# Kernel optimization log

Hardware: AMD Instinct MI355X
Metric: run time of the kernel (lower is better)

Reference implementation:

```python
import jax, jax.numpy as jnp
import numpy as np

N_NODES = 10000
N_EDGES = 160000


def setup_inputs() -> dict:
    key = jax.random.key(0)
    ks = jax.random.split(key, 12)
    B, N, DIN, DH, DOUT, L = 8, N_NODES, 512, 256, 3, 6
    s = lambda *d: 1.0 / np.sqrt(d[-2])
    return {
        "x": jax.random.normal(ks[0], (B, N, DIN), jnp.float32),
        "edge_src": jax.random.randint(ks[1], (N_EDGES,), 0, N, jnp.int32),
        "edge_dst": jax.random.randint(ks[2], (N_EDGES,), 0, N, jnp.int32),
        "edge_w": jax.random.uniform(ks[3], (N_EDGES,), jnp.float32) / 16.0,  # ~row-normalized
        "W_in": jax.random.normal(ks[4], (DIN, DH), jnp.float32) * s(DIN, DH),
        "LW_in": jax.random.normal(ks[5], (DIN, DH), jnp.float32) * s(DIN, DH),
        "b_in": jnp.zeros((DH,), jnp.float32),
        "W_blk": jax.random.normal(ks[6], (L, 2, DH, DH), jnp.float32) * s(DH, DH),
        "LW_blk": jax.random.normal(ks[7], (L, 2, DH, DH), jnp.float32) * s(DH, DH),
        "b_blk": jnp.zeros((L, 2, DH), jnp.float32),
        "W_out": jax.random.normal(ks[8], (DH, DOUT), jnp.float32) * s(DH, DOUT),
        "LW_out": jax.random.normal(ks[9], (DH, DOUT), jnp.float32) * s(DH, DOUT),
        "b_out": jnp.zeros((DOUT,), jnp.float32),
    }


def _gconv(x, esrc, edst, ew, W, LW, b):
    # x: [B,N,Din] -> [B,N,Dout]; out = A @ (x W) + x LW + b with sparse A
    support = jnp.einsum("bnd,de->bne", x, W)
    msgs = support[:, esrc, :] * ew[None, :, None]          # [B,E,Do]
    agg = jax.ops.segment_sum(msgs.transpose(1, 0, 2), edst,
                              num_segments=x.shape[1])       # [N,B,Do]
    agg = agg.transpose(1, 0, 2)                             # [B,N,Do]
    return agg + jnp.einsum("bnd,de->bne", x, LW) + b


def reference(x, edge_src, edge_dst, edge_w, W_in, LW_in, b_in,
              W_blk, LW_blk, b_blk, W_out, LW_out, b_out):
    h = _gconv(x, edge_src, edge_dst, edge_w, W_in, LW_in, b_in)
    for l in range(W_blk.shape[0]):  # GResBlock: two GConvs, residual, *0.5
        t = _gconv(h, edge_src, edge_dst, edge_w, W_blk[l, 0], LW_blk[l, 0], b_blk[l, 0])
        t = _gconv(t, edge_src, edge_dst, edge_w, W_blk[l, 1], LW_blk[l, 1], b_blk[l, 1])
        h = (h + t) * 0.5
    x_out = _gconv(h, edge_src, edge_dst, edge_w, W_out, LW_out, b_out)
    return (x_out, h)
```

## Files before the change

### kernel.cpp

```cpp
#include <hip/hip_runtime.h>

#define NN 10000
#define BB 8
#define MROWS 80000

typedef float f32x4 __attribute__((ext_vector_type(4)));
typedef unsigned int u32x4 __attribute__((ext_vector_type(4)));
typedef _Float16 f16;
typedef _Float16 f16x8 __attribute__((ext_vector_type(8)));

typedef __attribute__((address_space(1))) void as1_void;
typedef __attribute__((address_space(3))) void as3_void;

static __device__ __forceinline__ void gl_lds16(const void* g, void* l){
  __builtin_amdgcn_global_load_lds((as1_void*)g, (as3_void*)l, 16, 0, 0);
}

__global__ void k_count(const int* __restrict__ dst, int E, int* __restrict__ counts){
  int i = blockIdx.x * blockDim.x + threadIdx.x;
  if(i < E) atomicAdd(&counts[dst[i]], 1);
}

__global__ void k_scan(const int* __restrict__ counts, int* __restrict__ rp2){
  __shared__ int buf[1024];
  __shared__ int carry;
  const int t = threadIdx.x;
  if(t == 0){ carry = 0; rp2[0] = 0; }
  __syncthreads();
  for(int base = 0; base < NN; base += 1024){
    int v = (base + t < NN) ? ((counts[base + t] + 1) & ~1) : 0;
    buf[t] = v;
    __syncthreads();
    for(int off = 1; off < 1024; off <<= 1){
      int x = (t >= off) ? buf[t - off] : 0;
      __syncthreads();
      buf[t] += x;
      __syncthreads();
    }
    if(base + t < NN) rp2[base + t + 1] = carry + buf[t];
    __syncthreads();
    if(t == 0) carry += buf[1023];
    __syncthreads();
  }
}

__global__ void k_fill(const int* __restrict__ dst, int E, const int* __restrict__ rp2,
                       int* __restrict__ cursor, int* __restrict__ ci){
  int i = blockIdx.x * blockDim.x + threadIdx.x;
  if(i < E){
    int d = dst[i];
    int p = rp2[d] + atomicAdd(&cursor[d], 1);
    ci[p] = i;
  }
}

__global__ void k_sort_rows(const int* __restrict__ rp2, const int* __restrict__ cursor,
                            int* __restrict__ ci, unsigned int* __restrict__ ev,
                            const int* __restrict__ esrc, const float* __restrict__ ew){
  const int n = blockIdx.x * blockDim.x + threadIdx.x;
  if(n >= NN) return;
  const int s = rp2[n];
  const int deg = cursor[n];
  const int e = s + deg;
  for(int i = s; i < e - 1; ++i){
    int mj = i, mv = ci[i];
    for(int j = i + 1; j < e; ++j){
      int v = ci[j];
      if(v < mv){ mv = v; mj = j; }
    }
    ci[mj] = ci[i]; ci[i] = mv;
  }
  for(int p = s; p < e; ++p){
    int eid = ci[p];
    ev[2 * p]     = (unsigned int)esrc[eid];
    ev[2 * p + 1] = __float_as_uint(ew[eid]);
  }
  const int e2 = rp2[n + 1];
  for(int p = e; p < e2; ++p){
    ev[2 * p]     = 0u;
    ev[2 * p + 1] = 0u;
  }
}

__global__ void k_cvt(const float4* __restrict__ in, f16x8* __restrict__ out, int n8){
  int i = blockIdx.x * blockDim.x + threadIdx.x;
  if(i >= n8) return;
  float4 v0 = in[2 * i], v1 = in[2 * i + 1];
  f16x8 o;
  o[0] = (f16)v0.x; o[1] = (f16)v0.y; o[2] = (f16)v0.z; o[3] = (f16)v0.w;
  o[4] = (f16)v1.x; o[5] = (f16)v1.y; o[6] = (f16)v1.z; o[7] = (f16)v1.w;
  out[i] = o;
}

__global__ void k_pack_w(const float* __restrict__ Wi, const float* __restrict__ LWi,
                         const float* __restrict__ Wb, const float* __restrict__ LWb,
                         f16* __restrict__ dh){
  const int T0 = 512 * 512;
  const int TOT = T0 + 12 * 512 * 256;
  int i = blockIdx.x * blockDim.x + threadIdx.x;
  if(i >= TOT) return;
  float v;
  if(i < T0){
    int c = i >> 9, k = i & 511;
    v = (c < 256) ? Wi[k * 256 + c] : LWi[k * 256 + (c - 256)];
  } else {
    int j = i - T0;
    int li = j >> 17;
    int r = j & 131071;
    int c = r >> 8, k = r & 255;
    const float* src = (c < 256) ? (Wb + (size_t)li * 65536) : (LWb + (size_t)li * 65536);
    v = src[k * 256 + (c & 255)];
  }
  dh[i] = (f16)v;
}

__global__ __launch_bounds__(256) void k_gemm_dual(
    const f16* __restrict__ A, const f16* __restrict__ Bt,
    f16* __restrict__ Sup, f16* __restrict__ Loc, int K, int nblk)
{
  __shared__ char smem[40960];
  const int t = threadIdx.x;
  const int pid = blockIdx.x;
  const int q = nblk >> 3, r = nblk & 7;
  const int xcd = pid & 7, sl = pid >> 3;
  const int wg = (xcd < r ? xcd * (q + 1) : r * (q + 1) + (xcd - r) * q) + sl;
  const int m0 = (wg >> 1) << 6;
  const int by = wg & 1;
  const int n0 = by << 8;
  const int lane = t & 63, wv = t >> 6;
  const int rA = lane & 15, g = lane >> 4;
  f32x4 acc[4][4] = {};
  const int nsteps = K >> 5;
  const int rowt = t >> 2;
  const int csw  = (t & 3) ^ ((rowt >> 1) & 3);
  const int cbt  = csw << 3;

  auto STAGE = [&](int s, int buf){
    const int k0 = s << 5;
    const size_t aoff = (size_t)(m0 + rowt) * K + k0 + cbt;
    gl_lds16(A + aoff, smem + buf * 4096 + t * 16);
    #pragma unroll
    for(int qq = 0; qq < 4; ++qq){
      const size_t boff = (size_t)(n0 + qq * 64 + rowt) * K + k0 + cbt;
      gl_lds16(Bt + boff, smem + 8192 + buf * 16384 + qq * 4096 + t * 16);
    }
  };

  STAGE(0, 0);
  int cur = 0;
  const int slotx = (rA >> 1) & 3;

  for(int s = 0; s < nsteps; ++s){
    __builtin_amdgcn_sched_barrier(0);
    if(s + 1 < nsteps){
      STAGE(s + 1, cur ^ 1);
      asm volatile("s_waitcnt vmcnt(5)" ::: "memory");
    } else {
      asm volatile("s_waitcnt vmcnt(0)" ::: "memory");
    }
    __builtin_amdgcn_s_barrier();
    __builtin_amdgcn_sched_barrier(0);

    f16x8 av[4], bv[4];
    const f16* AsC = (const f16*)(smem + cur * 4096);
    const f16* BsC = (const f16*)(smem + 8192 + cur * 16384);
    #pragma unroll
    for(int mi = 0; mi < 4; ++mi){
      const int ao = (mi * 16 + rA) * 32 + ((g ^ slotx) << 3);
      av[mi] = *(const f16x8*)(AsC + ao);
    }
    #pragma unroll
    for(int ni = 0; ni < 4; ++ni){
      const int bo = wv * 2048 + (ni * 16 + rA) * 32 + ((g ^ slotx) << 3);
      bv[ni] = *(const f16x8*)(BsC + bo);
    }
    #pragma unroll
    for(int mi = 0; mi < 4; ++mi){
      #pragma unroll
      for(int ni = 0; ni < 4; ++ni){
        acc[mi][ni] = __builtin_amdgcn_mfma_f32_16x16x32_f16(av[mi], bv[ni], acc[mi][ni], 0, 0, 0);
      }
    }
    __builtin_amdgcn_sched_barrier(0);
    __builtin_amdgcn_s_barrier();
    cur ^= 1;
  }

  __syncthreads();
  f16* bounce = (f16*)smem;
  const int SP = 264;
  const int wn = wv << 6;
  #pragma unroll
  for(int mi = 0; mi < 4; ++mi){
    #pragma unroll
    for(int ni = 0; ni < 4; ++ni){
      const int col = wn + ni * 16 + rA;
      #pragma unroll
      for(int r2 = 0; r2 < 4; ++r2){
        bounce[(mi * 16 + g * 4 + r2) * SP + col] = (f16)acc[mi][ni][r2];
      }
    }
  }
  __syncthreads();
  f16* dstp = ((by == 0) ? Sup : Loc) + (size_t)m0 * 256;
  #pragma unroll
  for(int rr = 0; rr < 8; ++rr){
    const int e = rr * 2048 + t * 8;
    const int row = e >> 8, col = e & 255;
    const f16x8 v = *(const f16x8*)(bounce + row * SP + col);
    *(f16x8*)(dstp + e) = v;
  }
}

__global__ __launch_bounds__(256) void k_agg_q(
    const f16* __restrict__ Sup, const f16* __restrict__ Loc,
    const float* __restrict__ bias,
    const int* __restrict__ rp2, const unsigned int* __restrict__ ev,
    const f16* __restrict__ Hprev, f16* __restrict__ Hnext,
    float* __restrict__ hout, const int mode)
{
  const int pid = blockIdx.x;
  const int b = pid & 7;
  const int rest = pid >> 3;
  const int grp = rest % 313;
  const int qd  = rest / 313;
  const int t = threadIdx.x;
  const int j = t >> 3;
  const int l = t & 7;
  const int n = grp * 32 + j;
  if(n >= NN) return;
  const int d0 = (qd << 6) + (l << 3);
  const size_t rb = ((size_t)b * NN + n) * 256 + d0;
  float a[8];
  {
    const f16x8 lv = *(const f16x8*)(Loc + rb);
    float4 q0 = *(const float4*)(bias + d0);
    float4 q1 = *(const float4*)(bias + d0 + 4);
    a[0] = (float)lv[0] + q0.x; a[1] = (float)lv[1] + q0.y;
    a[2] = (float)lv[2] + q0.z; a[3] = (float)lv[3] + q0.w;
    a[4] = (float)lv[4] + q1.x; a[5] = (float)lv[5] + q1.y;
    a[6] = (float)lv[6] + q1.z; a[7] = (float)lv[7] + q1.w;
  }
  const int s = rp2[n], e = rp2[n + 1];
  const size_t bb = (size_t)b * NN * 256 + d0;
  for(int i = s; i < e; i += 2){
    const u32x4 ee = *(const u32x4*)(ev + 2 * i);
    const float w0 = __uint_as_float(ee[1]);
    const float w1 = __uint_as_float(ee[3]);
    const f16x8 h0 = *(const f16x8*)(Sup + bb + ((size_t)(int)ee[0]) * 256);
    const f16x8 h1 = *(const f16x8*)(Sup + bb + ((size_t)(int)ee[2]) * 256);
    #pragma unroll
    for(int d = 0; d < 8; ++d){
      a[d] = fmaf(w0, (float)h0[d], a[d]);
      a[d] = fmaf(w1, (float)h1[d], a[d]);
    }
  }
  if(mode >= 2){
    const f16x8 hp = *(const f16x8*)(Hprev + rb);
    #pragma unroll
    for(int d = 0; d < 8; ++d) a[d] = (a[d] + (float)hp[d]) * 0.5f;
  }
  if(mode == 3){
    f32x4 o0 = {a[0], a[1], a[2], a[3]};
    f32x4 o1 = {a[4], a[5], a[6], a[7]};
    *(f32x4*)(hout + rb) = o0;
    *(f32x4*)(hout + rb + 4) = o1;
    return;
  }
  f16x8 o;
  #pragma unroll
  for(int d = 0; d < 8; ++d) o[d] = (f16)a[d];
  *(f16x8*)(Hnext + rb) = o;
}

__global__ __launch_bounds__(256) void k_out_sup(const float* __restrict__ h,
    const float* __restrict__ Wo, float* __restrict__ sup3){
  const int gid = blockIdx.x * 4 + (threadIdx.x >> 6);
  const int lane = threadIdx.x & 63;
  if(gid >= MROWS) return;
  const float4 v = *(const float4*)(h + (size_t)gid * 256 + lane * 4);
  const float hv[4] = {v.x, v.y, v.z, v.w};
  float p0 = 0.f, p1 = 0.f, p2 = 0.f;
  #pragma unroll
  for(int j = 0; j < 4; ++j){
    const int k = lane * 4 + j;
    p0 = fmaf(hv[j], Wo[k * 3 + 0], p0);
    p1 = fmaf(hv[j], Wo[k * 3 + 1], p1);
    p2 = fmaf(hv[j], Wo[k * 3 + 2], p2);
  }
  #pragma unroll
  for(int off = 32; off; off >>= 1){
    p0 += __shfl_xor(p0, off, 64);
    p1 += __shfl_xor(p1, off, 64);
    p2 += __shfl_xor(p2, off, 64);
  }
  if(lane == 0){
    float* o = sup3 + (size_t)gid * 3;
    o[0] = p0; o[1] = p1; o[2] = p2;
  }
}

__global__ __launch_bounds__(256) void k_out_final(const float* __restrict__ h,
    const float* __restrict__ LWo, const float* __restrict__ bo,
    const int* __restrict__ rp2, const unsigned int* __restrict__ ev,
    const float* __restrict__ sup3, float* __restrict__ out){
  const int gid = blockIdx.x * 4 + (threadIdx.x >> 6);
  const int lane = threadIdx.x & 63;
  if(gid >= MROWS) return;
  const int b = gid / NN, n = gid % NN;
  const float4 v = *(const float4*)(h + (size_t)gid * 256 + lane * 4);
  const float hv[4] = {v.x, v.y, v.z, v.w};
  float p0 = 0.f, p1 = 0.f, p2 = 0.f;
  #pragma unroll
  for(int j = 0; j < 4; ++j){
    const int k = lane * 4 + j;
    p0 = fmaf(hv[j], LWo[k * 3 + 0], p0);
    p1 = fmaf(hv[j], LWo[k * 3 + 1], p1);
    p2 = fmaf(hv[j], LWo[k * 3 + 2], p2);
  }
  const int s = rp2[n], e = rp2[n + 1];
  for(int i = s + lane; i < e; i += 64){
    const int src = (int)ev[2 * i];
    const float w = __uint_as_float(ev[2 * i + 1]);
    const float* sp = sup3 + ((size_t)b * NN + src) * 3;
    p0 = fmaf(w, sp[0], p0);
    p1 = fmaf(w, sp[1], p1);
    p2 = fmaf(w, sp[2], p2);
  }
  #pragma unroll
  for(int off = 32; off; off >>= 1){
    p0 += __shfl_xor(p0, off, 64);
    p1 += __shfl_xor(p1, off, 64);
    p2 += __shfl_xor(p2, off, 64);
  }
  if(lane == 0){
    float* o = out + (size_t)gid * 3;
    o[0] = p0 + bo[0]; o[1] = p1 + bo[1]; o[2] = p2 + bo[2];
  }
}

extern "C" void kernel_launch(void* const* d_in, const int* in_sizes, int n_in,
                              void* d_out, int out_size, void* d_ws, size_t ws_size,
                              hipStream_t stream) {
  const float* x     = (const float*)d_in[0];
  const int*   esrc  = (const int*)d_in[1];
  const int*   edst  = (const int*)d_in[2];
  const float* ew    = (const float*)d_in[3];
  const float* W_in  = (const float*)d_in[4];
  const float* LW_in = (const float*)d_in[5];
  const float* b_in  = (const float*)d_in[6];
  const float* W_blk = (const float*)d_in[7];
  const float* LW_blk= (const float*)d_in[8];
  const float* b_blk = (const float*)d_in[9];
  const float* W_out = (const float*)d_in[10];
  const float* LW_out= (const float*)d_in[11];
  const float* b_out = (const float*)d_in[12];
  const int E = in_sizes[1];

  float* outF  = (float*)d_out;
  float* xout  = outF;
  float* hOut  = outF + 240000;
  f16* x16 = (f16*)hOut;

  char* ws = (char*)d_ws;
  size_t off = 0;
  auto alloc = [&](size_t bytes) -> char* {
    char* p = ws + off;
    off += (bytes + 255) & ~(size_t)255;
    return p;
  };
  const size_t HB = (size_t)20480000 * 2;
  f16* Ha  = (f16*)alloc(HB);
  f16* Hb  = (f16*)alloc(HB);
  f16* Sup = (f16*)alloc(HB);
  f16* Loc = (f16*)alloc(HB);
  const int WTOT = 512 * 512 + 12 * 512 * 256;
  f16* Wt = (f16*)alloc((size_t)WTOT * 2);
  float* sup3    = (float*)alloc((size_t)240000 * 4);
  int*   counts  = (int*)alloc((size_t)2 * NN * 4);
  int*   cursor  = counts + NN;
  int*   rp2     = (int*)alloc((size_t)(NN + 1) * 4);
  int*   ci      = (int*)alloc((size_t)(E + NN) * 4);
  unsigned int* ev = (unsigned int*)alloc((size_t)2 * (E + NN) * 4);
  (void)ws_size; (void)n_in; (void)out_size;

  hipMemsetAsync(counts, 0, (size_t)2 * NN * 4, stream);
  k_count<<<(E + 255) / 256, 256, 0, stream>>>(edst, E, counts);
  k_scan<<<1, 1024, 0, stream>>>(counts, rp2);
  k_fill<<<(E + 255) / 256, 256, 0, stream>>>(edst, E, rp2, cursor, ci);
  k_sort_rows<<<(NN + 255) / 256, 256, 0, stream>>>(rp2, cursor, ci, ev, esrc, ew);

  k_cvt<<<(5120000 + 255) / 256, 256, 0, stream>>>((const float4*)x, (f16x8*)x16, 5120000);
  k_pack_w<<<(WTOT + 255) / 256, 256, 0, stream>>>(W_in, LW_in, W_blk, LW_blk, Wt);

  const int NBLK = 2500;
  const int ABLK = 10016;
  k_gemm_dual<<<NBLK, 256, 0, stream>>>(x16, Wt, Sup, Loc, 512, NBLK);
  k_agg_q<<<ABLK, 256, 0, stream>>>(Sup, Loc, b_in, rp2, ev, Ha, Ha, xout, 0);

  const f16* Wm = Wt + 512 * 512;
  for(int l = 0; l < 6; ++l){
    const int li0 = 2 * l, li1 = 2 * l + 1;
    k_gemm_dual<<<NBLK, 256, 0, stream>>>(Ha, Wm + (size_t)li0 * 131072, Sup, Loc, 256, NBLK);
    k_agg_q<<<ABLK, 256, 0, stream>>>(Sup, Loc, b_blk + li0 * 256, rp2, ev, Ha, Hb, xout, 0);
    k_gemm_dual<<<NBLK, 256, 0, stream>>>(Hb, Wm + (size_t)li1 * 131072, Sup, Loc, 256, NBLK);
    k_agg_q<<<ABLK, 256, 0, stream>>>(Sup, Loc, b_blk + li1 * 256, rp2, ev, Ha, Ha, hOut, (l == 5) ? 3 : 2);
  }

  k_out_sup<<<MROWS / 4, 256, 0, stream>>>(hOut, W_out, sup3);
  k_out_final<<<MROWS / 4, 256, 0, stream>>>(hOut, LW_out, b_out, rp2, ev, sup3, xout);
}
```

Before: 1.464 ms.

## Add register-resident weight GEMM kernel for hidden-layer graph convolutions

Adds a persistent GEMM kernel for the 256-wide hidden layers. Each wave keeps a 64-column strip of the combined W|LW weight matrix in registers (32 f16x8 vectors) and loops over 16-row tiles of the activations. Results go through a small per-wave LDS bounce so the stores to Sup/Loc are coalesced. This removes the per-tile LDS staging and block-level syncs of the old dual GEMM. In exchange it uses much more register space, which lowers occupancy, and every wave reloads each A tile from global memory with no sharing across the 8 strips.

```diff
diff --git a/kernel.cpp b/kernel.cpp
--- a/kernel.cpp
+++ b/kernel.cpp
@@ -209,6 +209,66 @@
     const int row = e >> 8, col = e & 255;
     const f16x8 v = *(const f16x8*)(bounce + row * SP + col);
     *(f16x8*)(dstp + e) = v;
+  }
+}
+
+__global__ __launch_bounds__(256) void k_gemm_regB(
+    const f16* __restrict__ A, const f16* __restrict__ Bt,
+    f16* __restrict__ Sup, f16* __restrict__ Loc)
+{
+  __shared__ f16 bnc[4][16 * 72];
+  const int t = threadIdx.x;
+  const int wv = t >> 6, lane = t & 63;
+  const int gw = blockIdx.x * 4 + wv;
+  const int strip = gw & 7;
+  const int chunk = gw >> 3;
+  const int rA = lane & 15, g = lane >> 4;
+  f16* dst = (strip < 4) ? Sup : Loc;
+  const int dc0 = (strip & 3) << 6;
+
+  f16x8 breg[32];
+  {
+    const f16* bp = Bt + (size_t)((strip << 6) + rA) * 256 + g * 8;
+    #pragma unroll
+    for(int tt = 0; tt < 4; ++tt){
+      #pragma unroll
+      for(int ss = 0; ss < 8; ++ss){
+        breg[tt * 8 + ss] = *(const f16x8*)(bp + (size_t)tt * 16 * 256 + ss * 32);
+      }
+    }
+  }
+
+  const int rowrd = lane >> 2;
+  const int colrd = (lane & 3) << 4;
+  f16* mybnc = bnc[wv];
+
+  for(int mt = chunk; mt < 5000; mt += 256){
+    const f16* ap = A + (size_t)(mt * 16 + rA) * 256 + g * 8;
+    f16x8 av[8];
+    #pragma unroll
+    for(int ss = 0; ss < 8; ++ss) av[ss] = *(const f16x8*)(ap + ss * 32);
+    f32x4 acc[4] = {};
+    #pragma unroll
+    for(int ss = 0; ss < 8; ++ss){
+      #pragma unroll
+      for(int tt = 0; tt < 4; ++tt){
+        acc[tt] = __builtin_amdgcn_mfma_f32_16x16x32_f16(av[ss], breg[tt * 8 + ss], acc[tt], 0, 0, 0);
+      }
+    }
+    #pragma unroll
+    for(int tt = 0; tt < 4; ++tt){
+      #pragma unroll
+      for(int r2 = 0; r2 < 4; ++r2){
+        mybnc[(g * 4 + r2) * 72 + tt * 16 + rA] = (f16)acc[tt][r2];
+      }
+    }
+    asm volatile("s_waitcnt lgkmcnt(0)" ::: "memory");
+    const f16x8 v0 = *(const f16x8*)(mybnc + rowrd * 72 + colrd);
+    const f16x8 v1 = *(const f16x8*)(mybnc + rowrd * 72 + colrd + 8);
+    f16* dp = dst + (size_t)(mt * 16 + rowrd) * 256 + dc0 + colrd;
+    *(f16x8*)dp = v0;
+    *(f16x8*)(dp + 8) = v1;
+    asm volatile("s_waitcnt lgkmcnt(0)" ::: "memory");
   }
 }
 
@@ -394,6 +454,7 @@
   k_pack_w<<<(WTOT + 255) / 256, 256, 0, stream>>>(W_in, LW_in, W_blk, LW_blk, Wt);
 
   const int NBLK = 2500;
+  const int GBLK = 512;
   const int ABLK = 10016;
   k_gemm_dual<<<NBLK, 256, 0, stream>>>(x16, Wt, Sup, Loc, 512, NBLK);
   k_agg_q<<<ABLK, 256, 0, stream>>>(Sup, Loc, b_in, rp2, ev, Ha, Ha, xout, 0);
@@ -401,9 +462,9 @@
   const f16* Wm = Wt + 512 * 512;
   for(int l = 0; l < 6; ++l){
     const int li0 = 2 * l, li1 = 2 * l + 1;
-    k_gemm_dual<<<NBLK, 256, 0, stream>>>(Ha, Wm + (size_t)li0 * 131072, Sup, Loc, 256, NBLK);
+    k_gemm_regB<<<GBLK, 256, 0, stream>>>(Ha, Wm + (size_t)li0 * 131072, Sup, Loc);
     k_agg_q<<<ABLK, 256, 0, stream>>>(Sup, Loc, b_blk + li0 * 256, rp2, ev, Ha, Hb, xout, 0);
-    k_gemm_dual<<<NBLK, 256, 0, stream>>>(Hb, Wm + (size_t)li1 * 131072, Sup, Loc, 256, NBLK);
+    k_gemm_regB<<<GBLK, 256, 0, stream>>>(Hb, Wm + (size_t)li1 * 131072, Sup, Loc);
     k_agg_q<<<ABLK, 256, 0, stream>>>(Sup, Loc, b_blk + li1 * 256, rp2, ev, Ha, Ha, hOut, (l == 5) ? 3 : 2);
   }
 
```

Measured after the change: 1.652 ms. +12.9%, slower.

## Map GEMM blocks by batch to XCD and single-pass scan

Applied to the files above, without the earlier changes.

The dual GEMM now assigns work so that block index mod 8 selects the batch, keeping each batch's rows on one XCD. This matches the aggregation kernel's batch-per-XCD mapping and should improve L2 reuse between the GEMM and the aggregation. Per-batch tiles of 64 rows need padding at the batch boundary: row indices are clamped for loads, stores are masked, and the grid grows to 2512 blocks. The row-pointer scan also becomes a single 1024-thread pass, with each thread summing 10 counts serially, replacing ten chunked scans.

```diff
diff --git a/kernel.cpp b/kernel.cpp
--- a/kernel.cpp
+++ b/kernel.cpp
@@ -23,24 +23,31 @@
 
 __global__ void k_scan(const int* __restrict__ counts, int* __restrict__ rp2){
   __shared__ int buf[1024];
-  __shared__ int carry;
   const int t = threadIdx.x;
-  if(t == 0){ carry = 0; rp2[0] = 0; }
+  int loc[10];
+  int sum = 0;
+  const int base = t * 10;
+  #pragma unroll
+  for(int i = 0; i < 10; ++i){
+    const int idx = base + i;
+    const int v = (idx < NN) ? ((counts[idx] + 1) & ~1) : 0;
+    sum += v;
+    loc[i] = sum;
+  }
+  buf[t] = sum;
   __syncthreads();
-  for(int base = 0; base < NN; base += 1024){
-    int v = (base + t < NN) ? ((counts[base + t] + 1) & ~1) : 0;
-    buf[t] = v;
+  for(int off = 1; off < 1024; off <<= 1){
+    const int x = (t >= off) ? buf[t - off] : 0;
     __syncthreads();
-    for(int off = 1; off < 1024; off <<= 1){
-      int x = (t >= off) ? buf[t - off] : 0;
-      __syncthreads();
-      buf[t] += x;
-      __syncthreads();
-    }
-    if(base + t < NN) rp2[base + t + 1] = carry + buf[t];
+    buf[t] += x;
     __syncthreads();
-    if(t == 0) carry += buf[1023];
-    __syncthreads();
+  }
+  const int pre = (t == 0) ? 0 : buf[t - 1];
+  if(t == 0) rp2[0] = 0;
+  #pragma unroll
+  for(int i = 0; i < 10; ++i){
+    const int idx = base + i;
+    if(idx < NN) rp2[idx + 1] = pre + loc[i];
   }
 }
 
@@ -116,16 +123,16 @@
 
 __global__ __launch_bounds__(256) void k_gemm_dual(
     const f16* __restrict__ A, const f16* __restrict__ Bt,
-    f16* __restrict__ Sup, f16* __restrict__ Loc, int K, int nblk)
+    f16* __restrict__ Sup, f16* __restrict__ Loc, int K)
 {
   __shared__ char smem[40960];
   const int t = threadIdx.x;
   const int pid = blockIdx.x;
-  const int q = nblk >> 3, r = nblk & 7;
-  const int xcd = pid & 7, sl = pid >> 3;
-  const int wg = (xcd < r ? xcd * (q + 1) : r * (q + 1) + (xcd - r) * q) + sl;
-  const int m0 = (wg >> 1) << 6;
-  const int by = wg & 1;
+  const int b = pid & 7;
+  const int rest = pid >> 3;
+  const int by = rest & 1;
+  const int mt = rest >> 1;
+  const int mbase = mt << 6;
   const int n0 = by << 8;
   const int lane = t & 63, wv = t >> 6;
   const int rA = lane & 15, g = lane >> 4;
@@ -134,11 +141,13 @@
   const int rowt = t >> 2;
   const int csw  = (t & 3) ^ ((rowt >> 1) & 3);
   const int cbt  = csw << 3;
+  const int rl   = mbase + rowt;
+  const int rc   = (rl < NN) ? rl : (NN - 1);
+  const size_t arow = ((size_t)b * NN + rc) * K;
 
   auto STAGE = [&](int s, int buf){
     const int k0 = s << 5;
-    const size_t aoff = (size_t)(m0 + rowt) * K + k0 + cbt;
-    gl_lds16(A + aoff, smem + buf * 4096 + t * 16);
+    gl_lds16(A + arow + k0 + cbt, smem + buf * 4096 + t * 16);
     #pragma unroll
     for(int qq = 0; qq < 4; ++qq){
       const size_t boff = (size_t)(n0 + qq * 64 + rowt) * K + k0 + cbt;
@@ -202,13 +211,15 @@
     }
   }
   __syncthreads();
-  f16* dstp = ((by == 0) ? Sup : Loc) + (size_t)m0 * 256;
+  f16* dstp = ((by == 0) ? Sup : Loc) + ((size_t)b * NN + mbase) * 256;
   #pragma unroll
   for(int rr = 0; rr < 8; ++rr){
     const int e = rr * 2048 + t * 8;
     const int row = e >> 8, col = e & 255;
-    const f16x8 v = *(const f16x8*)(bounce + row * SP + col);
-    *(f16x8*)(dstp + e) = v;
+    if(mbase + row < NN){
+      const f16x8 v = *(const f16x8*)(bounce + row * SP + col);
+      *(f16x8*)(dstp + e) = v;
+    }
   }
 }
 
@@ -393,17 +404,17 @@
   k_cvt<<<(5120000 + 255) / 256, 256, 0, stream>>>((const float4*)x, (f16x8*)x16, 5120000);
   k_pack_w<<<(WTOT + 255) / 256, 256, 0, stream>>>(W_in, LW_in, W_blk, LW_blk, Wt);
 
-  const int NBLK = 2500;
+  const int NBLK = 2512;
   const int ABLK = 10016;
-  k_gemm_dual<<<NBLK, 256, 0, stream>>>(x16, Wt, Sup, Loc, 512, NBLK);
+  k_gemm_dual<<<NBLK, 256, 0, stream>>>(x16, Wt, Sup, Loc, 512);
   k_agg_q<<<ABLK, 256, 0, stream>>>(Sup, Loc, b_in, rp2, ev, Ha, Ha, xout, 0);
 
   const f16* Wm = Wt + 512 * 512;
   for(int l = 0; l < 6; ++l){
     const int li0 = 2 * l, li1 = 2 * l + 1;
-    k_gemm_dual<<<NBLK, 256, 0, stream>>>(Ha, Wm + (size_t)li0 * 131072, Sup, Loc, 256, NBLK);
+    k_gemm_dual<<<NBLK, 256, 0, stream>>>(Ha, Wm + (size_t)li0 * 131072, Sup, Loc, 256);
     k_agg_q<<<ABLK, 256, 0, stream>>>(Sup, Loc, b_blk + li0 * 256, rp2, ev, Ha, Hb, xout, 0);
-    k_gemm_dual<<<NBLK, 256, 0, stream>>>(Hb, Wm + (size_t)li1 * 131072, Sup, Loc, 256, NBLK);
+    k_gemm_dual<<<NBLK, 256, 0, stream>>>(Hb, Wm + (size_t)li1 * 131072, Sup, Loc, 256);
     k_agg_q<<<ABLK, 256, 0, stream>>>(Sup, Loc, b_blk + li1 * 256, rp2, ev, Ha, Ha, hOut, (l == 5) ? 3 : 2);
   }
 
```

Result: no change. 1.453 ms, median of 2 (-0.7%).
